# Kernel optimization log

Measured on AMD Instinct MI355X. Metric: run time of the kernel, lower is better.

Reference implementation:

```python
import jax, jax.numpy as jnp
import numpy as np

N0, N1, N2 = 100000, 50000, 10000
E1, E2 = 1600000, 320000
D = 128


def setup_inputs() -> dict:
    key = jax.random.key(0)
    ks = jax.random.split(key, 9)
    return {
        "x": jax.random.normal(ks[0], (N0, D), dtype=jnp.float32),
        "ew1": jax.random.uniform(ks[1], (E1,), dtype=jnp.float32),
        "ew2": jax.random.uniform(ks[2], (E2,), dtype=jnp.float32),
        "W": jax.random.normal(ks[3], (D, D), dtype=jnp.float32) * (1.0 / np.sqrt(D)),
        "b": jax.random.normal(ks[4], (D,), dtype=jnp.float32) * 0.01,
        "e1_src": jax.random.randint(ks[5], (E1,), 0, N0),
        "e1_dst": jax.random.randint(ks[6], (E1,), 0, N1),
        "e2_src": jax.random.randint(ks[7], (E2,), 0, N1),
        "e2_dst": jax.random.randint(ks[8], (E2,), 0, N2),
    }


def _spmm_block(h, src, dst, ew, num_dst):
    # u_mul_e + sum: m_e = h[src_e] * ew_e, reduced by sum onto dst nodes
    msgs = h[src] * ew[:, None]  # [E, D]
    return jax.ops.segment_sum(msgs, dst, num_segments=num_dst)


def reference(x, ew1, ew2, W, b, e1_src, e1_dst, e2_src, e2_dst):
    h = _spmm_block(x, e1_src, e1_dst, ew1, N1)   # block 1: [N1, D]
    h = _spmm_block(h, e2_src, e2_dst, ew2, N2)   # block 2: [N2, D]
    return h @ W.T + b                            # Linear(emb_dim, emb_dim)
```

## Files before the change

kernel.cpp:

```cpp
#include <hip/hip_runtime.h>

#define DD 128

constexpr int cN0 = 100000, cN1 = 50000, cN2 = 10000;
constexpr int NB1c = (cN1 + 31) / 32;
constexpr int NB2c = (cN2 + 15) / 16;
constexpr int CAP1 = 2048;
constexpr int CAP2 = 1024;

typedef unsigned long long ull;

__device__ __forceinline__ float bf_lo(unsigned int u) {
  return __uint_as_float(u << 16);
}
__device__ __forceinline__ float bf_hi(unsigned int u) {
  return __uint_as_float(u & 0xFFFF0000u);
}
__device__ __forceinline__ unsigned int pack_bf2(float a, float b) {
  unsigned int ua = __float_as_uint(a), ub = __float_as_uint(b);
  ua += 0x7FFFu + ((ua >> 16) & 1u);
  ub += 0x7FFFu + ((ub >> 16) & 1u);
  return (ua >> 16) | (ub & 0xFFFF0000u);
}

#define PAY_GATHER(PK, VX, VY)                                       \
  {                                                                  \
    int s_ = ((int)(unsigned int)(PK)) >> 5;                         \
    unsigned int v_ = h_in[(size_t)s_ * 64 + lane];                  \
    float w_ = __uint_as_float((unsigned int)((PK) >> 32));          \
    VX += bf_lo(v_) * w_;                                            \
    VY += bf_hi(v_) * w_;                                            \
  }

__global__ __launch_bounds__(256) void cvt_bf16_kernel(
    const float* __restrict__ in, unsigned int* __restrict__ outp, long long n8) {
  long long i = (long long)blockIdx.x * 256 + threadIdx.x;
  if (i >= n8) return;
  const float4* f4 = reinterpret_cast<const float4*>(in) + i * 2;
  float4 a = f4[0];
  float4 b = f4[1];
  uint4 o;
  o.x = pack_bf2(a.x, a.y);
  o.y = pack_bf2(a.z, a.w);
  o.z = pack_bf2(b.x, b.y);
  o.w = pack_bf2(b.z, b.w);
  reinterpret_cast<uint4*>(outp)[i] = o;
}

__global__ __launch_bounds__(256) void wt_kernel(
    const float* __restrict__ W, float* __restrict__ WT) {
  int idx = blockIdx.x * 256 + threadIdx.x;
  int c = idx >> 7;
  int d = idx & 127;
  WT[d * DD + c] = W[idx];
}

__global__ __launch_bounds__(1024) void passA_kernel(
    const int* __restrict__ d1, int E1, int nA1, int* __restrict__ bh1, int nblk1,
    const int* __restrict__ d2, int E2, int* __restrict__ bh2, int nblk2) {
  __shared__ int hist[NB1c];
  int lb = blockIdx.x;
  const int* dst; int E, NB, nblk, sh; int* bh;
  if (lb < nA1) { dst = d1; E = E1; NB = NB1c; nblk = nblk1; bh = bh1; sh = 5; }
  else { lb -= nA1; dst = d2; E = E2; NB = NB2c; nblk = nblk2; bh = bh2; sh = 4; }

  int t = threadIdx.x;
  for (int i = t; i < NB; i += 1024) hist[i] = 0;
  __syncthreads();

  int eb = lb * 4096;
#pragma unroll
  for (int r = 0; r < 4; ++r) {
    int e = eb + r * 1024 + t;
    if (e < E) atomicAdd(&hist[dst[e] >> sh], 1);
  }
  __syncthreads();
  for (int i = t; i < NB; i += 1024) bh[(size_t)i * nblk + lb] = hist[i];
}

__global__ __launch_bounds__(256) void scan_blk2_kernel(
    const int* __restrict__ cnt1, int n1, int* __restrict__ ofs1, int* __restrict__ bsum1, int nb1,
    const int* __restrict__ cnt2, int n2, int* __restrict__ ofs2, int* __restrict__ bsum2) {
  const int* cnt; int n; int* ofs; int* bsum; int lb;
  if ((int)blockIdx.x < nb1) { cnt = cnt1; n = n1; ofs = ofs1; bsum = bsum1; lb = blockIdx.x; }
  else                       { cnt = cnt2; n = n2; ofs = ofs2; bsum = bsum2; lb = blockIdx.x - nb1; }

  __shared__ int tsum[256];
  int t = threadIdx.x;
  int base = lb * 4096 + t * 16;
  bool in = (base + 16 <= n);

  int v[16];
  if (in) {
    const int4* p4 = reinterpret_cast<const int4*>(cnt + base);
    int4 a = p4[0], b = p4[1], c = p4[2], d = p4[3];
    v[0]=a.x; v[1]=a.y; v[2]=a.z; v[3]=a.w;
    v[4]=b.x; v[5]=b.y; v[6]=b.z; v[7]=b.w;
    v[8]=c.x; v[9]=c.y; v[10]=c.z; v[11]=c.w;
    v[12]=d.x; v[13]=d.y; v[14]=d.z; v[15]=d.w;
  } else {
#pragma unroll
    for (int k = 0; k < 16; ++k) v[k] = 0;
  }
#pragma unroll
  for (int k = 1; k < 16; ++k) v[k] += v[k - 1];

  tsum[t] = v[15];
  __syncthreads();
  for (int d_ = 1; d_ < 256; d_ <<= 1) {
    int x = (t >= d_) ? tsum[t - d_] : 0;
    __syncthreads();
    tsum[t] += x;
    __syncthreads();
  }
  int ex = (t == 0) ? 0 : tsum[t - 1];

  if (in) {
    int4* q = reinterpret_cast<int4*>(ofs + base);
    q[0] = make_int4(ex,         ex + v[0],  ex + v[1],  ex + v[2]);
    q[1] = make_int4(ex + v[3],  ex + v[4],  ex + v[5],  ex + v[6]);
    q[2] = make_int4(ex + v[7],  ex + v[8],  ex + v[9],  ex + v[10]);
    q[3] = make_int4(ex + v[11], ex + v[12], ex + v[13], ex + v[14]);
  }
  if (t == 255) bsum[lb] = tsum[255];
}

__global__ __launch_bounds__(1024) void scan_bsum2_kernel(
    int* __restrict__ bsum1, int nb1, int* __restrict__ bsum2, int nb2) {
  int* bsum; int nb;
  if (blockIdx.x == 0) { bsum = bsum1; nb = nb1; }
  else                 { bsum = bsum2; nb = nb2; }

  __shared__ int part[1024];
  int t = threadIdx.x;
  int orig = (t < nb) ? bsum[t] : 0;
  part[t] = orig;
  __syncthreads();
  for (int d_ = 1; d_ < 1024; d_ <<= 1) {
    int x = (t >= d_) ? part[t - d_] : 0;
    __syncthreads();
    part[t] += x;
    __syncthreads();
  }
  if (t < nb) bsum[t] = part[t] - orig;
}

__global__ __launch_bounds__(1024) void passB_kernel(
    const int* __restrict__ d1, const int* __restrict__ s1, const float* __restrict__ w1,
    int E1, int nA1, const int* __restrict__ S1, const int* __restrict__ bs1,
    int nblk1, ull* __restrict__ coarse1,
    const int* __restrict__ d2, const int* __restrict__ s2, const float* __restrict__ w2,
    int E2, const int* __restrict__ S2, const int* __restrict__ bs2,
    int nblk2, ull* __restrict__ coarse2) {
  __shared__ int cnt[NB1c];
  __shared__ int lscan[NB1c];
  __shared__ int cellst[NB1c];
  __shared__ int part[1024];
  __shared__ ull pay[4096];
  __shared__ unsigned short bkt_of[4096];

  int lb = blockIdx.x;
  const int* dst; const int* src; const float* ew;
  int E, NB, nblk, sh, msk; const int* S; const int* bs; ull* coarse;
  if (lb < nA1) {
    dst = d1; src = s1; ew = w1; E = E1; NB = NB1c; nblk = nblk1;
    S = S1; bs = bs1; coarse = coarse1; sh = 5; msk = 31;
  } else {
    lb -= nA1;
    dst = d2; src = s2; ew = w2; E = E2; NB = NB2c; nblk = nblk2;
    S = S2; bs = bs2; coarse = coarse2; sh = 4; msk = 15;
  }

  int t = threadIdx.x;
  int eb = lb * 4096;
  int ecount = E - eb; if (ecount > 4096) ecount = 4096;

  for (int i = t; i < NB; i += 1024) cnt[i] = 0;
  __syncthreads();

  ull pk0 = 0, pk1 = 0, pk2 = 0, pk3 = 0;
  int bk0 = -1, bk1 = -1, bk2 = -1, bk3 = -1;
#define LOADE(R, PK, BK)                                              \
  {                                                                   \
    int e = eb + (R) * 1024 + t;                                      \
    if (e < E) {                                                      \
      int d_ = dst[e];                                                \
      BK = d_ >> sh;                                                  \
      PK = ((ull)__float_as_uint(ew[e]) << 32) |                      \
           (unsigned int)((src[e] << 5) | (d_ & msk));                \
      atomicAdd(&cnt[BK], 1);                                         \
    }                                                                 \
  }
  LOADE(0, pk0, bk0) LOADE(1, pk1, bk1) LOADE(2, pk2, bk2) LOADE(3, pk3, bk3)
#undef LOADE
  __syncthreads();

  int i0 = 2 * t, i1 = 2 * t + 1;
  int c0 = (i0 < NB) ? cnt[i0] : 0;
  int c1 = (i1 < NB) ? cnt[i1] : 0;
  part[t] = c0 + c1;
  __syncthreads();
  for (int d_ = 1; d_ < 1024; d_ <<= 1) {
    int x = (t >= d_) ? part[t - d_] : 0;
    __syncthreads();
    part[t] += x;
    __syncthreads();
  }
  int ex = (t == 0) ? 0 : part[t - 1];
  if (i0 < NB) lscan[i0] = ex;
  if (i1 < NB) lscan[i1] = ex + c0;
  __syncthreads();

  for (int i = t; i < NB; i += 1024) {
    size_t idx = (size_t)i * nblk + lb;
    cellst[i] = S[idx] + bs[idx >> 12];
    cnt[i] = lscan[i];
  }
  __syncthreads();

#define PLACE(PK, BK)                                                 \
  if (BK >= 0) {                                                      \
    int pos = atomicAdd(&cnt[BK], 1);                                 \
    pay[pos] = PK;                                                    \
    bkt_of[pos] = (unsigned short)(BK);                               \
  }
  PLACE(pk0, bk0) PLACE(pk1, bk1) PLACE(pk2, bk2) PLACE(pk3, bk3)
#undef PLACE
  __syncthreads();

#pragma unroll
  for (int r = 0; r < 4; ++r) {
    int p = r * 1024 + t;
    if (p < ecount) {
      int b_ = bkt_of[p];
      int addr = cellst[b_] + (p - lscan[b_]);
      __builtin_nontemporal_store(pay[p], coarse + addr);
    }
  }
}

__global__ __launch_bounds__(256) void bucket_spmm1_kernel(
    const unsigned int* __restrict__ h_in,
    const int* __restrict__ S, const int* __restrict__ bs, int nblk,
    const ull* __restrict__ coarse, int E,
    unsigned int* __restrict__ h1b) {
  __shared__ ull pay[CAP1];
  __shared__ int h32[32], c32[32], binofs[32];
  int b = blockIdx.x;
  int t = threadIdx.x;
  int wid = t >> 6, lane = t & 63;

  size_t i0 = (size_t)b * nblk;
  int base = S[i0] + bs[i0 >> 12];
  int end;
  if (b == NB1c - 1) end = E;
  else {
    size_t i1 = (size_t)(b + 1) * nblk;
    end = S[i1] + bs[i1 >> 12];
  }
  int count = end - base;

  if (count <= CAP1) {
    if (t < 32) { h32[t] = 0; c32[t] = 0; }
    __syncthreads();
    for (int i = base + t; i < end; i += 256)
      atomicAdd(&h32[(int)(unsigned int)coarse[i] & 31], 1);
    __syncthreads();
    if (t == 0) {
      int run = 0;
#pragma unroll
      for (int k = 0; k < 32; ++k) { binofs[k] = run; run += h32[k]; }
    }
    __syncthreads();
    for (int i = base + t; i < end; i += 256) {
      ull pk = coarse[i];
      int dl = (int)(unsigned int)pk & 31;
      int rk = atomicAdd(&c32[dl], 1);
      pay[binofs[dl] + rk] = pk;
    }
    __syncthreads();

#pragma unroll
    for (int r = 0; r < 8; ++r) {
      int dl = wid * 8 + r;
      int row = b * 32 + dl;
      if (row >= cN1) break;
      int lo = binofs[dl], hi = lo + h32[dl];
      float accx = 0.f, accy = 0.f, ax1 = 0.f, ay1 = 0.f;
      int j = lo;
      for (; j + 8 <= hi; j += 8) {
        ull p0 = pay[j],     p1 = pay[j + 1], p2 = pay[j + 2], p3 = pay[j + 3];
        ull p4 = pay[j + 4], p5 = pay[j + 5], p6 = pay[j + 6], p7 = pay[j + 7];
        PAY_GATHER(p0, accx, accy) PAY_GATHER(p1, ax1, ay1)
        PAY_GATHER(p2, accx, accy) PAY_GATHER(p3, ax1, ay1)
        PAY_GATHER(p4, accx, accy) PAY_GATHER(p5, ax1, ay1)
        PAY_GATHER(p6, accx, accy) PAY_GATHER(p7, ax1, ay1)
      }
      for (; j < hi; ++j) { ull p0 = pay[j]; PAY_GATHER(p0, accx, accy) }
      h1b[(size_t)row * 64 + lane] = pack_bf2(accx + ax1, accy + ay1);
    }
  } else {
    for (int r = 0; r < 8; ++r) {
      int dl = wid * 8 + r;
      int row = b * 32 + dl;
      if (row >= cN1) break;
      float accx = 0.f, accy = 0.f;
      for (int i = base; i < end; ++i) {
        ull pk = coarse[i];
        if (((int)(unsigned int)pk & 31) == dl) { PAY_GATHER(pk, accx, accy) }
      }
      h1b[(size_t)row * 64 + lane] = pack_bf2(accx, accy);
    }
  }
}

__global__ __launch_bounds__(256) void bucket_spmm2_linear_kernel(
    const unsigned int* __restrict__ h_in,
    const int* __restrict__ S, const int* __restrict__ bs, int nblk,
    const ull* __restrict__ coarse, int E,
    const float* __restrict__ WT,
    const float* __restrict__ bias,
    float* __restrict__ out) {
  __shared__ ull pay[CAP2];
  __shared__ float hrow[16][DD];
  __shared__ int h16[16], c16[16], binofs[16];
  int b = blockIdx.x;
  int t = threadIdx.x;
  int wid = t >> 6, lane = t & 63;

  size_t i0 = (size_t)b * nblk;
  int base = S[i0] + bs[i0 >> 12];
  int end;
  if (b == NB2c - 1) end = E;
  else {
    size_t i1 = (size_t)(b + 1) * nblk;
    end = S[i1] + bs[i1 >> 12];
  }
  int count = end - base;

  if (count <= CAP2) {
    if (t < 16) { h16[t] = 0; c16[t] = 0; }
    __syncthreads();
    for (int i = base + t; i < end; i += 256)
      atomicAdd(&h16[(int)(unsigned int)coarse[i] & 15], 1);
    __syncthreads();
    if (t == 0) {
      int run = 0;
#pragma unroll
      for (int k = 0; k < 16; ++k) { binofs[k] = run; run += h16[k]; }
    }
    __syncthreads();
    for (int i = base + t; i < end; i += 256) {
      ull pk = coarse[i];
      int dl = (int)(unsigned int)pk & 15;
      int rk = atomicAdd(&c16[dl], 1);
      pay[binofs[dl] + rk] = pk;
    }
    __syncthreads();

#pragma unroll
    for (int r = 0; r < 4; ++r) {
      int dl = wid * 4 + r;
      int lo = binofs[dl], hi = lo + h16[dl];
      float accx = 0.f, accy = 0.f, ax1 = 0.f, ay1 = 0.f;
      int j = lo;
      for (; j + 8 <= hi; j += 8) {
        ull p0 = pay[j],     p1 = pay[j + 1], p2 = pay[j + 2], p3 = pay[j + 3];
        ull p4 = pay[j + 4], p5 = pay[j + 5], p6 = pay[j + 6], p7 = pay[j + 7];
        PAY_GATHER(p0, accx, accy) PAY_GATHER(p1, ax1, ay1)
        PAY_GATHER(p2, accx, accy) PAY_GATHER(p3, ax1, ay1)
        PAY_GATHER(p4, accx, accy) PAY_GATHER(p5, ax1, ay1)
        PAY_GATHER(p6, accx, accy) PAY_GATHER(p7, ax1, ay1)
      }
      for (; j < hi; ++j) { ull p0 = pay[j]; PAY_GATHER(p0, accx, accy) }
      float2 hv; hv.x = accx + ax1; hv.y = accy + ay1;
      *reinterpret_cast<float2*>(&hrow[dl][2 * lane]) = hv;
    }
  } else {
    for (int r = 0; r < 4; ++r) {
      int dl = wid * 4 + r;
      float accx = 0.f, accy = 0.f;
      for (int i = base; i < end; ++i) {
        ull pk = coarse[i];
        if (((int)(unsigned int)pk & 15) == dl) { PAY_GATHER(pk, accx, accy) }
      }
      float2 hv; hv.x = accx; hv.y = accy;
      *reinterpret_cast<float2*>(&hrow[dl][2 * lane]) = hv;
    }
  }

  float2 bb = reinterpret_cast<const float2*>(bias)[lane];
  float a0[4], a1[4];
#pragma unroll
  for (int r = 0; r < 4; ++r) { a0[r] = bb.x; a1[r] = bb.y; }

  const float* hbase = &hrow[wid * 4][0];
#pragma unroll 4
  for (int d = 0; d < DD; ++d) {
    float2 wv = *reinterpret_cast<const float2*>(WT + (size_t)d * DD + 2 * lane);
#pragma unroll
    for (int r = 0; r < 4; ++r) {
      float h = hbase[r * DD + d];
      a0[r] += h * wv.x;
      a1[r] += h * wv.y;
    }
  }
#pragma unroll
  for (int r = 0; r < 4; ++r) {
    int row = b * 16 + wid * 4 + r;
    if (row < cN2) {
      float2 o; o.x = a0[r]; o.y = a1[r];
      reinterpret_cast<float2*>(out + (size_t)row * DD)[lane] = o;
    }
  }
}

static inline size_t align256(size_t x) { return (x + 255) & ~size_t(255); }
static inline int pad16i(int x) { return (x + 15) & ~15; }

extern "C" void kernel_launch(void* const* d_in, const int* in_sizes, int n_in,
                              void* d_out, int out_size, void* d_ws, size_t ws_size,
                              hipStream_t stream) {
  const float* x   = (const float*)d_in[0];
  const float* ew1 = (const float*)d_in[1];
  const float* ew2 = (const float*)d_in[2];
  const float* W   = (const float*)d_in[3];
  const float* b   = (const float*)d_in[4];
  const int* e1_src = (const int*)d_in[5];
  const int* e1_dst = (const int*)d_in[6];
  const int* e2_src = (const int*)d_in[7];
  const int* e2_dst = (const int*)d_in[8];
  float* out = (float*)d_out;

  int E1 = in_sizes[1];
  int E2 = in_sizes[2];

  int nA1 = (E1 + 4095) / 4096;
  int nA2 = (E2 + 4095) / 4096;
  int nc1 = pad16i(NB1c * nA1);
  int nc2 = pad16i(NB2c * nA2);
  int nbs1 = (nc1 + 4095) / 4096;
  int nbs2 = (nc2 + 4095) / 4096;

  char* p = (char*)d_ws;
  unsigned int* xb  = (unsigned int*)p;  p += align256((size_t)cN0 * DD * 2);
  unsigned int* h1b = (unsigned int*)p;  p += align256((size_t)cN1 * DD * 2);
  float* WT = (float*)p;                 p += align256((size_t)DD * DD * 4);
  int* bh1 = (int*)p;                    p += align256((size_t)(nc1 + 16) * 4);
  int* bh2 = (int*)p;                    p += align256((size_t)(nc2 + 16) * 4);
  int* S1  = (int*)p;                    p += align256((size_t)(nc1 + 16) * 4);
  int* S2  = (int*)p;                    p += align256((size_t)(nc2 + 16) * 4);
  int* bsum1 = (int*)p;                  p += align256(4096);
  int* bsum2 = (int*)p;                  p += align256(4096);
  ull* coarse1 = (ull*)p;                p += align256((size_t)E1 * 8);
  ull* coarse2 = (ull*)p;                p += align256((size_t)E2 * 8);

  {
    long long n8 = (long long)cN0 * DD / 8;
    cvt_bf16_kernel<<<(int)((n8 + 255) / 256), 256, 0, stream>>>(x, xb, n8);
  }
  wt_kernel<<<64, 256, 0, stream>>>(W, WT);

  passA_kernel<<<nA1 + nA2, 1024, 0, stream>>>(
      e1_dst, E1, nA1, bh1, nA1, e2_dst, E2, bh2, nA2);

  scan_blk2_kernel<<<nbs1 + nbs2, 256, 0, stream>>>(
      bh1, nc1, S1, bsum1, nbs1, bh2, nc2, S2, bsum2);
  scan_bsum2_kernel<<<2, 1024, 0, stream>>>(bsum1, nbs1, bsum2, nbs2);

  passB_kernel<<<nA1 + nA2, 1024, 0, stream>>>(
      e1_dst, e1_src, ew1, E1, nA1, S1, bsum1, nA1, coarse1,
      e2_dst, e2_src, ew2, E2, S2, bsum2, nA2, coarse2);

  bucket_spmm1_kernel<<<NB1c, 256, 0, stream>>>(
      xb, S1, bsum1, nA1, coarse1, E1, h1b);

  bucket_spmm2_linear_kernel<<<NB2c, 256, 0, stream>>>(
      h1b, S2, bsum2, nA2, coarse2, E2, WT, b, out);
}
```

Before: 151.3 us.

## Merge prep kernels and fold block-sum scan into consumer kernels

Result: no change. 148.8 us (-1.6%).

```diff
diff --git a/kernel.cpp b/kernel.cpp
--- a/kernel.cpp
+++ b/kernel.cpp
@@ -32,50 +32,71 @@
     VY += bf_hi(v_) * w_;                                            \
   }
 
-__global__ __launch_bounds__(256) void cvt_bf16_kernel(
-    const float* __restrict__ in, unsigned int* __restrict__ outp, long long n8) {
-  long long i = (long long)blockIdx.x * 256 + threadIdx.x;
-  if (i >= n8) return;
-  const float4* f4 = reinterpret_cast<const float4*>(in) + i * 2;
-  float4 a = f4[0];
-  float4 b = f4[1];
-  uint4 o;
-  o.x = pack_bf2(a.x, a.y);
-  o.y = pack_bf2(a.z, a.w);
-  o.z = pack_bf2(b.x, b.y);
-  o.w = pack_bf2(b.z, b.w);
-  reinterpret_cast<uint4*>(outp)[i] = o;
-}
-
-__global__ __launch_bounds__(256) void wt_kernel(
-    const float* __restrict__ W, float* __restrict__ WT) {
-  int idx = blockIdx.x * 256 + threadIdx.x;
-  int c = idx >> 7;
-  int d = idx & 127;
-  WT[d * DD + c] = W[idx];
-}
-
-__global__ __launch_bounds__(1024) void passA_kernel(
-    const int* __restrict__ d1, int E1, int nA1, int* __restrict__ bh1, int nblk1,
-    const int* __restrict__ d2, int E2, int* __restrict__ bh2, int nblk2) {
+__device__ __forceinline__ void wave_scan_bsum(
+    const int* __restrict__ raw, int nb, int* lds_out, int tid) {
+  if (tid < 64) {
+    int carry = 0;
+    for (int base = 0; base < nb; base += 64) {
+      int i = base + tid;
+      int orig = (i < nb) ? raw[i] : 0;
+      int v = orig;
+      for (int d = 1; d < 64; d <<= 1) {
+        int u = __shfl_up(v, d);
+        if (tid >= d) v += u;
+      }
+      if (i < nb) lds_out[i] = carry + v - orig;
+      carry += __shfl(v, 63);
+    }
+  }
+}
+
+__global__ __launch_bounds__(1024) void prep_kernel(
+    const int* __restrict__ d1, int E1, int nA1, int* __restrict__ bh1,
+    const int* __restrict__ d2, int E2, int nA2, int* __restrict__ bh2,
+    const float* __restrict__ x, unsigned int* __restrict__ xb, long long n8,
+    int ncvt, const float* __restrict__ W, float* __restrict__ WT) {
   __shared__ int hist[NB1c];
-  int lb = blockIdx.x;
-  const int* dst; int E, NB, nblk, sh; int* bh;
-  if (lb < nA1) { dst = d1; E = E1; NB = NB1c; nblk = nblk1; bh = bh1; sh = 5; }
-  else { lb -= nA1; dst = d2; E = E2; NB = NB2c; nblk = nblk2; bh = bh2; sh = 4; }
-
+  int blk = blockIdx.x;
   int t = threadIdx.x;
-  for (int i = t; i < NB; i += 1024) hist[i] = 0;
-  __syncthreads();
-
-  int eb = lb * 4096;
-#pragma unroll
-  for (int r = 0; r < 4; ++r) {
-    int e = eb + r * 1024 + t;
-    if (e < E) atomicAdd(&hist[dst[e] >> sh], 1);
-  }
-  __syncthreads();
-  for (int i = t; i < NB; i += 1024) bh[(size_t)i * nblk + lb] = hist[i];
+  int nA = nA1 + nA2;
+
+  if (blk < nA) {
+    const int* dst; int E, NB, nblk, sh; int* bh; int lb;
+    if (blk < nA1) { dst = d1; E = E1; NB = NB1c; nblk = nA1; bh = bh1; sh = 5; lb = blk; }
+    else { dst = d2; E = E2; NB = NB2c; nblk = nA2; bh = bh2; sh = 4; lb = blk - nA1; }
+
+    for (int i = t; i < NB; i += 1024) hist[i] = 0;
+    __syncthreads();
+
+    int eb = lb * 4096;
+#pragma unroll
+    for (int r = 0; r < 4; ++r) {
+      int e = eb + r * 1024 + t;
+      if (e < E) atomicAdd(&hist[dst[e] >> sh], 1);
+    }
+    __syncthreads();
+    for (int i = t; i < NB; i += 1024) bh[(size_t)i * nblk + lb] = hist[i];
+  } else if (blk < nA + ncvt) {
+    long long i = (long long)(blk - nA) * 1024 + t;
+    if (i < n8) {
+      const float4* f4 = reinterpret_cast<const float4*>(x) + i * 2;
+      float4 a = f4[0];
+      float4 b = f4[1];
+      uint4 o;
+      o.x = pack_bf2(a.x, a.y);
+      o.y = pack_bf2(a.z, a.w);
+      o.z = pack_bf2(b.x, b.y);
+      o.w = pack_bf2(b.z, b.w);
+      reinterpret_cast<uint4*>(xb)[i] = o;
+    }
+  } else {
+    int idx = (blk - nA - ncvt) * 1024 + t;
+    if (idx < DD * DD) {
+      int c = idx >> 7;
+      int d = idx & 127;
+      WT[d * DD + c] = W[idx];
+    }
+  }
 }
 
 __global__ __launch_bounds__(256) void scan_blk2_kernel(
@@ -125,56 +146,38 @@
   if (t == 255) bsum[lb] = tsum[255];
 }
 
-__global__ __launch_bounds__(1024) void scan_bsum2_kernel(
-    int* __restrict__ bsum1, int nb1, int* __restrict__ bsum2, int nb2) {
-  int* bsum; int nb;
-  if (blockIdx.x == 0) { bsum = bsum1; nb = nb1; }
-  else                 { bsum = bsum2; nb = nb2; }
-
-  __shared__ int part[1024];
-  int t = threadIdx.x;
-  int orig = (t < nb) ? bsum[t] : 0;
-  part[t] = orig;
-  __syncthreads();
-  for (int d_ = 1; d_ < 1024; d_ <<= 1) {
-    int x = (t >= d_) ? part[t - d_] : 0;
-    __syncthreads();
-    part[t] += x;
-    __syncthreads();
-  }
-  if (t < nb) bsum[t] = part[t] - orig;
-}
-
 __global__ __launch_bounds__(1024) void passB_kernel(
     const int* __restrict__ d1, const int* __restrict__ s1, const float* __restrict__ w1,
-    int E1, int nA1, const int* __restrict__ S1, const int* __restrict__ bs1,
+    int E1, int nA1, const int* __restrict__ S1, const int* __restrict__ bs1, int nbs1,
     int nblk1, ull* __restrict__ coarse1,
     const int* __restrict__ d2, const int* __restrict__ s2, const float* __restrict__ w2,
-    int E2, const int* __restrict__ S2, const int* __restrict__ bs2,
+    int E2, const int* __restrict__ S2, const int* __restrict__ bs2, int nbs2,
     int nblk2, ull* __restrict__ coarse2) {
   __shared__ int cnt[NB1c];
   __shared__ int lscan[NB1c];
   __shared__ int cellst[NB1c];
   __shared__ int part[1024];
+  __shared__ int sbs[192];
   __shared__ ull pay[4096];
   __shared__ unsigned short bkt_of[4096];
 
   int lb = blockIdx.x;
   const int* dst; const int* src; const float* ew;
-  int E, NB, nblk, sh, msk; const int* S; const int* bs; ull* coarse;
+  int E, NB, nblk, sh, msk, nbs; const int* S; const int* bs; ull* coarse;
   if (lb < nA1) {
     dst = d1; src = s1; ew = w1; E = E1; NB = NB1c; nblk = nblk1;
-    S = S1; bs = bs1; coarse = coarse1; sh = 5; msk = 31;
+    S = S1; bs = bs1; nbs = nbs1; coarse = coarse1; sh = 5; msk = 31;
   } else {
     lb -= nA1;
     dst = d2; src = s2; ew = w2; E = E2; NB = NB2c; nblk = nblk2;
-    S = S2; bs = bs2; coarse = coarse2; sh = 4; msk = 15;
+    S = S2; bs = bs2; nbs = nbs2; coarse = coarse2; sh = 4; msk = 15;
   }
 
   int t = threadIdx.x;
   int eb = lb * 4096;
   int ecount = E - eb; if (ecount > 4096) ecount = 4096;
 
+  wave_scan_bsum(bs, nbs, sbs, t);
   for (int i = t; i < NB; i += 1024) cnt[i] = 0;
   __syncthreads();
 
@@ -213,7 +216,7 @@
 
   for (int i = t; i < NB; i += 1024) {
     size_t idx = (size_t)i * nblk + lb;
-    cellst[i] = S[idx] + bs[idx >> 12];
+    cellst[i] = S[idx] + sbs[idx >> 12];
     cnt[i] = lscan[i];
   }
   __syncthreads();
@@ -241,28 +244,31 @@
 
 __global__ __launch_bounds__(256) void bucket_spmm1_kernel(
     const unsigned int* __restrict__ h_in,
-    const int* __restrict__ S, const int* __restrict__ bs, int nblk,
+    const int* __restrict__ S, const int* __restrict__ bs, int nbs, int nblk,
     const ull* __restrict__ coarse, int E,
     unsigned int* __restrict__ h1b) {
   __shared__ ull pay[CAP1];
   __shared__ int h32[32], c32[32], binofs[32];
+  __shared__ int sbs[192];
   int b = blockIdx.x;
   int t = threadIdx.x;
   int wid = t >> 6, lane = t & 63;
 
+  wave_scan_bsum(bs, nbs, sbs, t);
+  if (t < 32) { h32[t] = 0; c32[t] = 0; }
+  __syncthreads();
+
   size_t i0 = (size_t)b * nblk;
-  int base = S[i0] + bs[i0 >> 12];
+  int base = S[i0] + sbs[i0 >> 12];
   int end;
   if (b == NB1c - 1) end = E;
   else {
     size_t i1 = (size_t)(b + 1) * nblk;
-    end = S[i1] + bs[i1 >> 12];
+    end = S[i1] + sbs[i1 >> 12];
   }
   int count = end - base;
 
   if (count <= CAP1) {
-    if (t < 32) { h32[t] = 0; c32[t] = 0; }
-    __syncthreads();
     for (int i = base + t; i < end; i += 256)
       atomicAdd(&h32[(int)(unsigned int)coarse[i] & 31], 1);
     __syncthreads();
@@ -316,7 +322,7 @@
 
 __global__ __launch_bounds__(256) void bucket_spmm2_linear_kernel(
     const unsigned int* __restrict__ h_in,
-    const int* __restrict__ S, const int* __restrict__ bs, int nblk,
+    const int* __restrict__ S, const int* __restrict__ bs, int nbs, int nblk,
     const ull* __restrict__ coarse, int E,
     const float* __restrict__ WT,
     const float* __restrict__ bias,
@@ -324,23 +330,26 @@
   __shared__ ull pay[CAP2];
   __shared__ float hrow[16][DD];
   __shared__ int h16[16], c16[16], binofs[16];
+  __shared__ int sbs[64];
   int b = blockIdx.x;
   int t = threadIdx.x;
   int wid = t >> 6, lane = t & 63;
 
+  wave_scan_bsum(bs, nbs, sbs, t);
+  if (t < 16) { h16[t] = 0; c16[t] = 0; }
+  __syncthreads();
+
   size_t i0 = (size_t)b * nblk;
-  int base = S[i0] + bs[i0 >> 12];
+  int base = S[i0] + sbs[i0 >> 12];
   int end;
   if (b == NB2c - 1) end = E;
   else {
     size_t i1 = (size_t)(b + 1) * nblk;
-    end = S[i1] + bs[i1 >> 12];
+    end = S[i1] + sbs[i1 >> 12];
   }
   int count = end - base;
 
   if (count <= CAP2) {
-    if (t < 16) { h16[t] = 0; c16[t] = 0; }
-    __syncthreads();
     for (int i = base + t; i < end; i += 256)
       atomicAdd(&h16[(int)(unsigned int)coarse[i] & 15], 1);
     __syncthreads();
@@ -442,6 +451,10 @@
   int nbs1 = (nc1 + 4095) / 4096;
   int nbs2 = (nc2 + 4095) / 4096;
 
+  long long n8 = (long long)cN0 * DD / 8;
+  int ncvt = (int)((n8 + 1023) / 1024);
+  int nwt  = (DD * DD + 1023) / 1024;
+
   char* p = (char*)d_ws;
   unsigned int* xb  = (unsigned int*)p;  p += align256((size_t)cN0 * DD * 2);
   unsigned int* h1b = (unsigned int*)p;  p += align256((size_t)cN1 * DD * 2);
@@ -455,26 +468,20 @@
   ull* coarse1 = (ull*)p;                p += align256((size_t)E1 * 8);
   ull* coarse2 = (ull*)p;                p += align256((size_t)E2 * 8);
 
-  {
-    long long n8 = (long long)cN0 * DD / 8;
-    cvt_bf16_kernel<<<(int)((n8 + 255) / 256), 256, 0, stream>>>(x, xb, n8);
-  }
-  wt_kernel<<<64, 256, 0, stream>>>(W, WT);
-
-  passA_kernel<<<nA1 + nA2, 1024, 0, stream>>>(
-      e1_dst, E1, nA1, bh1, nA1, e2_dst, E2, bh2, nA2);
+  prep_kernel<<<nA1 + nA2 + ncvt + nwt, 1024, 0, stream>>>(
+      e1_dst, E1, nA1, bh1, e2_dst, E2, nA2, bh2,
+      x, xb, n8, ncvt, W, WT);
 
   scan_blk2_kernel<<<nbs1 + nbs2, 256, 0, stream>>>(
       bh1, nc1, S1, bsum1, nbs1, bh2, nc2, S2, bsum2);
-  scan_bsum2_kernel<<<2, 1024, 0, stream>>>(bsum1, nbs1, bsum2, nbs2);
 
   passB_kernel<<<nA1 + nA2, 1024, 0, stream>>>(
-      e1_dst, e1_src, ew1, E1, nA1, S1, bsum1, nA1, coarse1,
-      e2_dst, e2_src, ew2, E2, S2, bsum2, nA2, coarse2);
+      e1_dst, e1_src, ew1, E1, nA1, S1, bsum1, nbs1, nA1, coarse1,
+      e2_dst, e2_src, ew2, E2, S2, bsum2, nbs2, nA2, coarse2);
 
   bucket_spmm1_kernel<<<NB1c, 256, 0, stream>>>(
-      xb, S1, bsum1, nA1, coarse1, E1, h1b);
+      xb, S1, bsum1, nbs1, nA1, coarse1, E1, h1b);
 
   bucket_spmm2_linear_kernel<<<NB2c, 256, 0, stream>>>(
-      h1b, S2, bsum2, nA2, coarse2, E2, WT, b, out);
-}
+      h1b, S2, bsum2, nbs2, nA2, coarse2, E2, WT, b, out);
+}
```
